# Optimization experiments

Hardware: AMD Instinct MI355X
Metric: run time of the kernel (lower is better)

## Reference

```python
import jax, jax.numpy as jnp
import numpy as np

B, T, D, E = 4, 2048, 1024, 4096


def setup_inputs() -> dict:
    key = jax.random.key(0)
    ks = jax.random.split(key, 6)
    s = 0.02
    return {
        "x": jax.random.normal(ks[0], (B, T, D), jnp.float32),
        "W1": jax.random.normal(ks[1], (E, D), jnp.float32) * s,
        "b1": jnp.zeros((E,), jnp.float32),
        "W2": jax.random.normal(ks[2], (E, D), jnp.float32) * s,
        "b2": jnp.zeros((E,), jnp.float32),
        "Wg": jax.random.normal(ks[3], (2 * E, E), jnp.float32) * s,
        "bg": jnp.zeros((2 * E,), jnp.float32),
        "Wo": jax.random.normal(ks[4], (D, E), jnp.float32) * s,
        "bo": jnp.zeros((D,), jnp.float32),
    }


def _log_g(x):
    # log of g(x) where g(x) = x+0.5 for x>=0 else sigmoid(x)
    return jnp.where(x >= 0, jnp.log(jax.nn.relu(x) + 0.5), -jax.nn.softplus(-x))


def _min_gru(x_in, Wg, bg):
    # x_in: [B,T,E]; single linear -> (gate, candidate), log-space parallel scan, h0 = 0
    gh = jnp.einsum('bte,fe->btf', x_in, Wg) + bg
    gate, hidden = jnp.split(gh, 2, axis=-1)
    log_coeffs = -jax.nn.softplus(gate)          # log(1 - z)
    log_z = -jax.nn.softplus(-gate)              # log z
    log_values = log_z + _log_g(hidden)          # log(z * g(h_tilde))
    a_star = jnp.cumsum(log_coeffs, axis=1)      # Heinsen associative scan
    log_h = a_star + jax.lax.cumlogsumexp(log_values - a_star, axis=1)
    return jnp.exp(log_h)


def reference(x, W1, b1, W2, b2, Wg, bg, Wo, bo):
    x_in = jax.nn.silu(jnp.einsum('btd,ed->bte', x, W1) + b1)
    x_skip = jax.nn.silu(jnp.einsum('btd,ed->bte', x, W2) + b2)
    h = _min_gru(x_in, Wg, bg)
    return jnp.einsum('bte,de->btd', x_skip + h, Wo) + bo
```

## Files before the change

kernel.cpp:

```cpp
#include <hip/hip_runtime.h>
#include <cstdint>
#include <cstddef>

constexpr int CB  = 4;
constexpr int CT  = 2048;
constexpr int CD  = 1024;
constexpr int CE  = 4096;
constexpr int CM  = CB * CT;
constexpr int CN2E = 2 * CE;
constexpr int NCHUNK = 32;
constexpr int CLEN = CT / NCHUNK;

typedef float  f32x4  __attribute__((ext_vector_type(4)));
typedef __bf16 bf16x8 __attribute__((ext_vector_type(8)));

__device__ __forceinline__ unsigned short f2bf(float f) {
  unsigned int u = __float_as_uint(f);
  unsigned int r = u + 0x7FFFu + ((u >> 16) & 1u);
  return (unsigned short)(r >> 16);
}
__device__ __forceinline__ float bf2f(unsigned short h) {
  return __uint_as_float(((unsigned int)h) << 16);
}

__global__ __launch_bounds__(256) void k_f2bf4(const float* __restrict__ in,
                                               unsigned short* __restrict__ out, int n4) {
  int i = blockIdx.x * 256 + threadIdx.x;
  if (i >= n4) return;
  float4 v = ((const float4*)in)[i];
  ushort4 o;
  o.x = f2bf(v.x); o.y = f2bf(v.y); o.z = f2bf(v.z); o.w = f2bf(v.w);
  ((ushort4*)out)[i] = o;
}

__device__ __forceinline__ void gll16(const unsigned short* g, void* l) {
  __builtin_amdgcn_global_load_lds(
      (const __attribute__((address_space(1))) void*)g,
      (__attribute__((address_space(3))) void*)l, 16, 0, 0);
}

template <int EPI>
__global__ __launch_bounds__(512, 2) void gemm256(
    const unsigned short* __restrict__ A,
    const unsigned short* __restrict__ Bw,
    const float* __restrict__ bias0,
    const float* __restrict__ bias1,
    void* __restrict__ out0,
    void* __restrict__ out1,
    int M, int N, int K, int lda, int ld0, int esplit) {
  extern __shared__ char lds[];

  const int nbn = N >> 8;
  const int nbm = M >> 8;
  const int nwg = nbm * nbn;
  int bid = blockIdx.x;
  int tau = (bid & 7) * (nwg >> 3) + (bid >> 3);
  const int gsz = nbm * 4;
  int gg  = tau / gsz;
  int rem = tau - gg * gsz;
  const int bm = rem >> 2;
  const int bn = gg * 4 + (rem & 3);

  const int tid  = threadIdx.x;
  const int lane = tid & 63;
  const int wv   = tid >> 6;
  const int wr   = wv >> 2;
  const int wc   = wv & 3;

  const int tp   = tid ^ ((tid >> 3) & 3);
  const int srow = tp >> 2;
  const int scol = (tp & 3) * 8;

  const unsigned short* Abase = A  + (size_t)bm * 256 * lda;
  const unsigned short* Bbase = Bw + (size_t)bn * 256 * (size_t)K;
  const int ldsw = wv * 1024;
  const int NT = K >> 5;

  auto stageA = [&](int t) {
    char* base = lds + (size_t)(t & 3) * 32768 + ldsw;
    const int kt = t * 32;
    gll16(Abase + (size_t)srow * lda + kt + scol,         base);
    gll16(Abase + (size_t)(srow + 128) * lda + kt + scol, base + 8192);
  };
  auto stageB = [&](int t) {
    char* base = lds + (size_t)(t & 3) * 32768 + 16384 + ldsw;
    const int kt = t * 32;
    gll16(Bbase + (size_t)srow * K + kt + scol,           base);
    gll16(Bbase + (size_t)(srow + 128) * K + kt + scol,   base + 8192);
  };

  const int lr = lane & 15, gq = lane >> 4;
  const int arow = wr * 128 + lr;
  const int aoff = arow * 64 + (gq ^ ((arow >> 1) & 3)) * 16;
  const int brow = wc * 64 + lr;
  const int boff = 16384 + brow * 64 + (gq ^ ((brow >> 1) & 3)) * 16;

  f32x4 acc[8][4];
#pragma unroll
  for (int m = 0; m < 8; m++)
#pragma unroll
    for (int n = 0; n < 4; n++) acc[m][n] = (f32x4){0.f, 0.f, 0.f, 0.f};

  stageA(0); stageB(0); stageA(1); stageB(1); stageA(2); stageB(2);

  for (int t = 0; t < NT; t++) {
    if (t < NT - 2)       asm volatile("s_waitcnt vmcnt(8)" ::: "memory");
    else if (t == NT - 2) asm volatile("s_waitcnt vmcnt(4)" ::: "memory");
    else                  asm volatile("s_waitcnt vmcnt(0)" ::: "memory");
    __builtin_amdgcn_sched_barrier(0);
    __builtin_amdgcn_s_barrier();
    __builtin_amdgcn_sched_barrier(0);

    const char* bufp = lds + (size_t)(t & 3) * 32768;
    bf16x8 af[4], bfr[4];
#pragma unroll
    for (int i = 0; i < 4; i++) af[i]  = *(const bf16x8*)(bufp + aoff + i * 1024);
#pragma unroll
    for (int i = 0; i < 4; i++) bfr[i] = *(const bf16x8*)(bufp + boff + i * 1024);
    if (t + 3 < NT) stageA(t + 3);
    __builtin_amdgcn_sched_barrier(0);
    __builtin_amdgcn_s_barrier();
    __builtin_amdgcn_sched_barrier(0);
    __builtin_amdgcn_s_setprio(1);
#pragma unroll
    for (int m = 0; m < 4; m++)
#pragma unroll
      for (int n = 0; n < 4; n++)
        acc[m][n] = __builtin_amdgcn_mfma_f32_16x16x32_bf16(af[m], bfr[n], acc[m][n], 0, 0, 0);
    __builtin_amdgcn_s_setprio(0);
    __builtin_amdgcn_sched_barrier(0);
    __builtin_amdgcn_s_barrier();
    __builtin_amdgcn_sched_barrier(0);
#pragma unroll
    for (int i = 0; i < 4; i++) af[i] = *(const bf16x8*)(bufp + aoff + (i + 4) * 1024);
    if (t + 3 < NT) stageB(t + 3);
    __builtin_amdgcn_sched_barrier(0);
    __builtin_amdgcn_s_barrier();
    __builtin_amdgcn_sched_barrier(0);
    __builtin_amdgcn_s_setprio(1);
#pragma unroll
    for (int m = 0; m < 4; m++)
#pragma unroll
      for (int n = 0; n < 4; n++)
        acc[m + 4][n] = __builtin_amdgcn_mfma_f32_16x16x32_bf16(af[m], bfr[n], acc[m + 4][n], 0, 0, 0);
    __builtin_amdgcn_s_setprio(0);
  }

  const int rb = bm * 256 + wr * 128 + (lane >> 4) * 4;
  const int cb = bn * 256 + wc * 64 + (lane & 15);
#pragma unroll
  for (int nf = 0; nf < 4; nf++) {
    const int col = cb + nf * 16;
    float bi;
    if (EPI == 0) bi = (col < esplit) ? bias0[col] : bias1[col - esplit];
    else          bi = bias0[col];
#pragma unroll
    for (int mf = 0; mf < 8; mf++) {
#pragma unroll
      for (int r = 0; r < 4; r++) {
        const int row = rb + mf * 16 + r;
        float v = acc[mf][nf][r] + bi;
        if (EPI == 0) {
          float sg = 1.f / (1.f + __expf(-v));
          unsigned short o = f2bf(v * sg);
          if (col < esplit) ((unsigned short*)out0)[(size_t)row * ld0 + col] = o;
          else              ((unsigned short*)out1)[(size_t)row * ld0 + (col - esplit)] = o;
        } else {
          unsigned short o;
          if (col < esplit) {
            float e = __expf(-fabsf(v));
            float inv = 1.f / (1.f + e);
            o = f2bf((v >= 0.f) ? e * inv : inv);
          } else {
            float gf;
            if (v >= 0.f) gf = v + 0.5f;
            else { float eh = __expf(v); gf = eh / (1.f + eh); }
            o = f2bf(gf);
          }
          ((unsigned short*)out0)[(size_t)row * ld0 + col] = o;
        }
      }
    }
  }
}

__global__ __launch_bounds__(256) void gemm_bt1(
    const unsigned short* __restrict__ A,
    const unsigned short* __restrict__ Bw,
    const float* __restrict__ bias0,
    float* __restrict__ out0,
    int M, int N, int K, int lda, int ld0) {
  __shared__ __align__(16) unsigned short As[128 * 32];
  __shared__ __align__(16) unsigned short Bs[128 * 32];

  const int nbn = N >> 7;
  const int nwg = (M >> 7) * nbn;
  int bid = blockIdx.x;
  bid = (bid & 7) * (nwg >> 3) + (bid >> 3);
  const int bm = bid / nbn;
  const int bn = bid - bm * nbn;

  const int tid  = threadIdx.x;
  const int lane = tid & 63;
  const int wv   = tid >> 6;
  const int wr   = wv >> 1;
  const int wc   = wv & 1;
  const int lrow = lane & 15;
  const int lk   = lane >> 4;

  const unsigned short* Abase = A  + (size_t)bm * 128 * lda;
  const unsigned short* Bbase = Bw + (size_t)bn * 128 * K;
  const int r0 = tid >> 2;
  const int c0 = (tid & 3) * 8;
  char* AsB = (char*)As + (size_t)wv * 1024;
  char* BsB = (char*)Bs + (size_t)wv * 1024;

  f32x4 acc[4][4];
#pragma unroll
  for (int m = 0; m < 4; m++)
#pragma unroll
    for (int n = 0; n < 4; n++) acc[m][n] = (f32x4){0.f, 0.f, 0.f, 0.f};

  for (int kt = 0; kt < K; kt += 32) {
    __syncthreads();
    gll16(Abase + (size_t)r0 * lda + kt + c0,        AsB);
    gll16(Abase + (size_t)(r0 + 64) * lda + kt + c0, AsB + 4096);
    gll16(Bbase + (size_t)r0 * K + kt + c0,          BsB);
    gll16(Bbase + (size_t)(r0 + 64) * K + kt + c0,   BsB + 4096);
    __syncthreads();

    const bf16x8* Av = (const bf16x8*)As;
    const bf16x8* Bv = (const bf16x8*)Bs;
    bf16x8 af[4], bfv[4];
#pragma unroll
    for (int m = 0; m < 4; m++) af[m]  = Av[(wr * 64 + m * 16 + lrow) * 4 + lk];
#pragma unroll
    for (int n = 0; n < 4; n++) bfv[n] = Bv[(wc * 64 + n * 16 + lrow) * 4 + lk];
#pragma unroll
    for (int m = 0; m < 4; m++)
#pragma unroll
      for (int n = 0; n < 4; n++)
        acc[m][n] = __builtin_amdgcn_mfma_f32_16x16x32_bf16(af[m], bfv[n], acc[m][n], 0, 0, 0);
  }

  const int rbase = bm * 128 + wr * 64 + (lane >> 4) * 4;
  const int cbase = bn * 128 + wc * 64 + (lane & 15);
#pragma unroll
  for (int n = 0; n < 4; n++) {
    const int col = cbase + n * 16;
    const float bi = bias0[col];
#pragma unroll
    for (int m = 0; m < 4; m++)
#pragma unroll
      for (int r = 0; r < 4; r++)
        out0[(size_t)(rbase + m * 16 + r) * ld0 + col] = acc[m][n][r] + bi;
  }
}

__global__ __launch_bounds__(256) void k_scan1(const unsigned short* __restrict__ ghc,
                                               float* __restrict__ Ac,
                                               float* __restrict__ Bc) {
  int tid = threadIdx.x;
  int lane = tid & 63, cw = tid >> 6;
  int bid = blockIdx.x;
  int eg = bid & 63;
  int cq = bid >> 6;
  int chunk = cq * 4 + cw;
  int e = eg * 64 + lane;
  const unsigned short* cp = ghc + (size_t)(chunk * CLEN) * CN2E + e;
  float h = 0.f, A = 1.f;
#pragma unroll 8
  for (int t = 0; t < CLEN; t++) {
    float c  = bf2f(cp[(size_t)t * CN2E]);
    float gf = bf2f(cp[(size_t)t * CN2E + CE]);
    float v  = (1.f - c) * gf;
    h = __builtin_fmaf(c, h, v);
    A *= c;
  }
  Ac[(size_t)chunk * CE + e] = A;
  Bc[(size_t)chunk * CE + e] = h;
}

__global__ __launch_bounds__(256) void k_scan2(const float* __restrict__ Ac,
                                               const float* __restrict__ Bc,
                                               float* __restrict__ Hs) {
  int e = blockIdx.x * 256 + threadIdx.x;
  float h = 0.f;
#pragma unroll
  for (int ch = 0; ch < NCHUNK; ch++) {
    Hs[(size_t)ch * CE + e] = h;
    h = __builtin_fmaf(Ac[(size_t)ch * CE + e], h, Bc[(size_t)ch * CE + e]);
  }
}

__global__ __launch_bounds__(256) void k_scan3(const unsigned short* __restrict__ ghc,
                                               const float* __restrict__ Hs,
                                               const unsigned short* __restrict__ xs,
                                               unsigned short* __restrict__ sp) {
  int tid = threadIdx.x;
  int lane = tid & 63, cw = tid >> 6;
  int bid = blockIdx.x;
  int eg = bid & 63;
  int cq = bid >> 6;
  int chunk = cq * 4 + cw;
  int e = eg * 64 + lane;
  float h = Hs[(size_t)chunk * CE + e];
  const unsigned short* cp  = ghc + (size_t)(chunk * CLEN) * CN2E + e;
  const unsigned short* xsp = xs  + (size_t)(chunk * CLEN) * CE + e;
  unsigned short*       spp = sp  + (size_t)(chunk * CLEN) * CE + e;
#pragma unroll 4
  for (int t = 0; t < CLEN; t++) {
    float c  = bf2f(cp[(size_t)t * CN2E]);
    float gf = bf2f(cp[(size_t)t * CN2E + CE]);
    float v  = (1.f - c) * gf;
    h = __builtin_fmaf(c, h, v);
    float s = h + bf2f(xsp[(size_t)t * CE]);
    spp[(size_t)t * CE] = f2bf(s);
  }
}

extern "C" void kernel_launch(void* const* d_in, const int* in_sizes, int n_in,
                              void* d_out, int out_size, void* d_ws, size_t ws_size,
                              hipStream_t stream) {
  const float* x  = (const float*)d_in[0];
  const float* W1 = (const float*)d_in[1];
  const float* b1 = (const float*)d_in[2];
  const float* W2 = (const float*)d_in[3];
  const float* b2 = (const float*)d_in[4];
  const float* Wg = (const float*)d_in[5];
  const float* bg = (const float*)d_in[6];
  const float* Wo = (const float*)d_in[7];
  const float* bo = (const float*)d_in[8];
  float* out = (float*)d_out;

  const size_t MB = 1024 * 1024;
  if (ws_size < 234 * MB) return;
  char* ws = (char*)d_ws;
  unsigned short* wgb   = (unsigned short*)(ws);
  unsigned short* wob   = (unsigned short*)(ws + 64 * MB);
  unsigned short* wcat  = (unsigned short*)(ws + 72 * MB);
  unsigned short* xb    = (unsigned short*)(ws + 88 * MB);
  unsigned short* ghc   = (unsigned short*)(ws + 72 * MB);
  unsigned short* xin   = (unsigned short*)(ws + 104 * MB);
  unsigned short* xskip = (unsigned short*)(ws + 168 * MB);
  float* Ac = (float*)(ws + 232 * MB);
  float* Bc = (float*)(ws + 232 * MB + 512 * 1024);
  float* Hs = (float*)(ws + 233 * MB);

  hipFuncSetAttribute(reinterpret_cast<const void*>(&gemm256<0>),
                      hipFuncAttributeMaxDynamicSharedMemorySize, 131072);
  hipFuncSetAttribute(reinterpret_cast<const void*>(&gemm256<2>),
                      hipFuncAttributeMaxDynamicSharedMemorySize, 131072);

  {
    int n4;
    n4 = CM * CD / 4;   k_f2bf4<<<n4 / 256, 256, 0, stream>>>(x,  xb,   n4);
    n4 = CE * CD / 4;   k_f2bf4<<<n4 / 256, 256, 0, stream>>>(W1, wcat, n4);
    n4 = CE * CD / 4;   k_f2bf4<<<n4 / 256, 256, 0, stream>>>(W2, wcat + (size_t)CE * CD, n4);
    n4 = CN2E * CE / 4; k_f2bf4<<<n4 / 256, 256, 0, stream>>>(Wg, wgb,  n4);
    n4 = CD * CE / 4;   k_f2bf4<<<n4 / 256, 256, 0, stream>>>(Wo, wob,  n4);
  }

  gemm256<0><<<(CM / 256) * (CN2E / 256), 512, 131072, stream>>>(
      xb, wcat, b1, b2, xin, xskip, CM, CN2E, CD, CD, CE, CE);

  for (int b = 0; b < CB; b++) {
    const unsigned short* xin_b = xin + (size_t)b * CT * CE;
    gemm256<2><<<(CT / 256) * (CN2E / 256), 512, 131072, stream>>>(
        xin_b, wgb, bg, nullptr, ghc, nullptr, CT, CN2E, CE, CE, CN2E, CE);
    k_scan1<<<512, 256, 0, stream>>>(ghc, Ac, Bc);
    k_scan2<<<CE / 256, 256, 0, stream>>>(Ac, Bc, Hs);
    k_scan3<<<512, 256, 0, stream>>>(ghc, Hs, xskip + (size_t)b * CT * CE,
                                     xin + (size_t)b * CT * CE);
  }

  gemm_bt1<<<(CM / 128) * (CD / 128), 256, 0, stream>>>(
      xin, wob, bo, out, CM, CD, CE, CE, CD);
}
```

Before: 978.9 us.

## Restructure GEMM mainloop to K=64 double-buffered tiles with 8-way XOR swizzle

The GEMM mainloop moves from a 4-stage ring of K=32 LDS tiles to a 2-stage double buffer of K=64 tiles. The LDS swizzle becomes an 8-way XOR over 128-byte rows. MFMA work is split into four phases, and next-tile A/B loads are issued during the first two. This halves the iteration count and the number of waitcnt/barrier sync points per K. In exchange, prefetch depth drops from three tiles ahead to one, which may expose more global-load latency.

Result: faster. 928.7 us (-5.1%).

```diff
diff --git a/kernel.cpp b/kernel.cpp
--- a/kernel.cpp
+++ b/kernel.cpp
@@ -67,33 +67,33 @@
   const int wr   = wv >> 2;
   const int wc   = wv & 3;
 
-  const int tp   = tid ^ ((tid >> 3) & 3);
-  const int srow = tp >> 2;
-  const int scol = (tp & 3) * 8;
+  const int sr  = tid >> 3;
+  const int sc8 = (((tid & 7) ^ (sr & 7)) * 8);
 
   const unsigned short* Abase = A  + (size_t)bm * 256 * lda;
   const unsigned short* Bbase = Bw + (size_t)bn * 256 * (size_t)K;
-  const int ldsw = wv * 1024;
-  const int NT = K >> 5;
+  const int NT = K >> 6;
 
   auto stageA = [&](int t) {
-    char* base = lds + (size_t)(t & 3) * 32768 + ldsw;
-    const int kt = t * 32;
-    gll16(Abase + (size_t)srow * lda + kt + scol,         base);
-    gll16(Abase + (size_t)(srow + 128) * lda + kt + scol, base + 8192);
+    char* base = lds + (size_t)(t & 1) * 65536 + wv * 1024;
+    const unsigned short* g = Abase + t * 64 + sc8;
+#pragma unroll
+    for (int q = 0; q < 4; q++)
+      gll16(g + (size_t)(q * 64 + sr) * lda, base + q * 8192);
   };
   auto stageB = [&](int t) {
-    char* base = lds + (size_t)(t & 3) * 32768 + 16384 + ldsw;
-    const int kt = t * 32;
-    gll16(Bbase + (size_t)srow * K + kt + scol,           base);
-    gll16(Bbase + (size_t)(srow + 128) * K + kt + scol,   base + 8192);
+    char* base = lds + (size_t)(t & 1) * 65536 + 32768 + wv * 1024;
+    const unsigned short* g = Bbase + t * 64 + sc8;
+#pragma unroll
+    for (int q = 0; q < 4; q++)
+      gll16(g + (size_t)(q * 64 + sr) * K, base + q * 8192);
   };
 
-  const int lr = lane & 15, gq = lane >> 4;
-  const int arow = wr * 128 + lr;
-  const int aoff = arow * 64 + (gq ^ ((arow >> 1) & 3)) * 16;
-  const int brow = wc * 64 + lr;
-  const int boff = 16384 + brow * 64 + (gq ^ ((brow >> 1) & 3)) * 16;
+  const int lr = lane & 15, lk = lane >> 4;
+  const int pk[2] = { ((lk)     ^ (lr & 7)) * 16,
+                      ((4 + lk) ^ (lr & 7)) * 16 };
+  const int aLaneB = (wr * 128 + lr) * 128;
+  const int bLaneB = 32768 + (wc * 64 + lr) * 128;
 
   f32x4 acc[8][4];
 #pragma unroll
@@ -101,49 +101,50 @@
 #pragma unroll
     for (int n = 0; n < 4; n++) acc[m][n] = (f32x4){0.f, 0.f, 0.f, 0.f};
 
-  stageA(0); stageB(0); stageA(1); stageB(1); stageA(2); stageB(2);
+  stageA(0); stageB(0);
+  asm volatile("s_waitcnt vmcnt(0)" ::: "memory");
+  __builtin_amdgcn_sched_barrier(0);
+  __builtin_amdgcn_s_barrier();
+  __builtin_amdgcn_sched_barrier(0);
 
   for (int t = 0; t < NT; t++) {
-    if (t < NT - 2)       asm volatile("s_waitcnt vmcnt(8)" ::: "memory");
-    else if (t == NT - 2) asm volatile("s_waitcnt vmcnt(4)" ::: "memory");
-    else                  asm volatile("s_waitcnt vmcnt(0)" ::: "memory");
+    const char* bp = lds + (size_t)(t & 1) * 65536;
+    bf16x8 bfr[2][4];
+
+#pragma unroll
+    for (int p = 0; p < 4; p++) {
+      bf16x8 aq[2][2];
+#pragma unroll
+      for (int q = 0; q < 2; q++)
+#pragma unroll
+        for (int ks = 0; ks < 2; ks++)
+          aq[q][ks] = *(const bf16x8*)(bp + aLaneB + (2 * p + q) * 2048 + pk[ks]);
+      if (p == 0) {
+#pragma unroll
+        for (int ks = 0; ks < 2; ks++)
+#pragma unroll
+          for (int nf = 0; nf < 4; nf++)
+            bfr[ks][nf] = *(const bf16x8*)(bp + bLaneB + nf * 2048 + pk[ks]);
+        if (t + 1 < NT) stageA(t + 1);
+      }
+      if (p == 1 && t + 1 < NT) stageB(t + 1);
+      __builtin_amdgcn_s_barrier();
+      __builtin_amdgcn_s_setprio(1);
+#pragma unroll
+      for (int ks = 0; ks < 2; ks++)
+#pragma unroll
+        for (int q = 0; q < 2; q++)
+#pragma unroll
+          for (int nf = 0; nf < 4; nf++)
+            acc[2 * p + q][nf] = __builtin_amdgcn_mfma_f32_16x16x32_bf16(
+                aq[q][ks], bfr[ks][nf], acc[2 * p + q][nf], 0, 0, 0);
+      __builtin_amdgcn_s_setprio(0);
+    }
+
+    asm volatile("s_waitcnt vmcnt(0)" ::: "memory");
     __builtin_amdgcn_sched_barrier(0);
     __builtin_amdgcn_s_barrier();
     __builtin_amdgcn_sched_barrier(0);
-
-    const char* bufp = lds + (size_t)(t & 3) * 32768;
-    bf16x8 af[4], bfr[4];
-#pragma unroll
-    for (int i = 0; i < 4; i++) af[i]  = *(const bf16x8*)(bufp + aoff + i * 1024);
-#pragma unroll
-    for (int i = 0; i < 4; i++) bfr[i] = *(const bf16x8*)(bufp + boff + i * 1024);
-    if (t + 3 < NT) stageA(t + 3);
-    __builtin_amdgcn_sched_barrier(0);
-    __builtin_amdgcn_s_barrier();
-    __builtin_amdgcn_sched_barrier(0);
-    __builtin_amdgcn_s_setprio(1);
-#pragma unroll
-    for (int m = 0; m < 4; m++)
-#pragma unroll
-      for (int n = 0; n < 4; n++)
-        acc[m][n] = __builtin_amdgcn_mfma_f32_16x16x32_bf16(af[m], bfr[n], acc[m][n], 0, 0, 0);
-    __builtin_amdgcn_s_setprio(0);
-    __builtin_amdgcn_sched_barrier(0);
-    __builtin_amdgcn_s_barrier();
-    __builtin_amdgcn_sched_barrier(0);
-#pragma unroll
-    for (int i = 0; i < 4; i++) af[i] = *(const bf16x8*)(bufp + aoff + (i + 4) * 1024);
-    if (t + 3 < NT) stageB(t + 3);
-    __builtin_amdgcn_sched_barrier(0);
-    __builtin_amdgcn_s_barrier();
-    __builtin_amdgcn_sched_barrier(0);
-    __builtin_amdgcn_s_setprio(1);
-#pragma unroll
-    for (int m = 0; m < 4; m++)
-#pragma unroll
-      for (int n = 0; n < 4; n++)
-        acc[m + 4][n] = __builtin_amdgcn_mfma_f32_16x16x32_bf16(af[m], bfr[n], acc[m + 4][n], 0, 0, 0);
-    __builtin_amdgcn_s_setprio(0);
   }
 
   const int rb = bm * 256 + wr * 128 + (lane >> 4) * 4;
```
